# Kernel tuning notes

Measured on AMD Instinct MI355X. Metric: run time of the kernel, lower is better.

Reference implementation:

```python
import jax, jax.numpy as jnp
import numpy as np

TOP_K = 2  # num_experts_per_tok


def setup_inputs() -> dict:
    key = jax.random.key(0)
    k1, k2, k3, k4 = jax.random.split(key, 4)
    T, H, I, E = 1024, 2048, 768, 8  # tokens, hidden, moe_intermediate, num_experts
    return {
        "hidden_states": jax.random.normal(k1, (T, H), jnp.float32),
        "gate_w": jax.random.normal(k2, (E, H), jnp.float32) * 0.02,      # router nn.Linear(H,E) weight
        "w_gate_up": jax.random.normal(k3, (E, 2 * I, H), jnp.float32) * 0.02,  # merged gate+up proj per expert
        "w_down": jax.random.normal(k4, (E, H, I), jnp.float32) * 0.02,   # down proj per expert
    }


def _moe(hidden_states, gate_w, w_gate_up, w_down):
    T, H = hidden_states.shape
    E = gate_w.shape[0]
    # router: softmax in fp32, then top-k, renormalize (matches _forward_local)
    logits = hidden_states @ gate_w.T                         # [T, E]
    probs = jax.nn.softmax(logits.astype(jnp.float32), axis=-1)
    top_w, top_i = jax.lax.top_k(probs, TOP_K)                # [T, K]
    top_w = top_w / jnp.sum(top_w, axis=-1, keepdims=True)
    top_w = top_w.astype(hidden_states.dtype)
    # per-token combine weight for each expert (top-k indices are unique per token)
    comb = jnp.zeros((T, E), hidden_states.dtype).at[
        jnp.arange(T)[:, None], top_i
    ].add(top_w)                                              # [T, E]

    def body(acc, xs):
        wgu, wd, cw = xs            # [2I,H], [H,I], [T]
        gu = hidden_states @ wgu.T  # [T, 2I]
        g, u = jnp.split(gu, 2, axis=-1)
        h = jax.nn.silu(g) * u      # SiluAndMul
        out = h @ wd.T              # [T, H]
        return acc + out * cw[:, None], None

    init = jnp.zeros_like(hidden_states)
    out, _ = jax.lax.scan(body, init, (w_gate_up, w_down, comb.T))
    return out


def reference(hidden_states, gate_w, w_gate_up, w_down):
    return _moe(hidden_states, gate_w, w_gate_up, w_down)
```

## Files before the change

### kernel.cpp

```cpp
#include <hip/hip_runtime.h>
#include <hip/hip_bf16.h>

typedef unsigned short u16;
typedef __bf16 bf16x8 __attribute__((ext_vector_type(8)));
typedef float f32x4 __attribute__((ext_vector_type(4)));

#define T_TOK 1024
#define HID   2048
#define IMM   768
#define NE    8
#define TWOI  1536

static __device__ __forceinline__ u16 f2bf(float f) {
  unsigned u = __float_as_uint(f);
  u += 0x7FFFu + ((u >> 16) & 1u);
  return (u16)(u >> 16);
}
static __device__ __forceinline__ float bf2f(u16 s) {
  return __uint_as_float(((unsigned)s) << 16);
}

__global__ __launch_bounds__(64) void router_kernel(
    const float* __restrict__ hid, const float* __restrict__ gw,
    int* __restrict__ cnt, int* __restrict__ tok_of, float* __restrict__ wslot)
{
  const int t = blockIdx.x;
  const int lane = threadIdx.x;
  float acc[NE];
#pragma unroll
  for (int e = 0; e < NE; ++e) acc[e] = 0.f;
  const float4* h4 = (const float4*)(hid + (long)t * HID);
#pragma unroll 2
  for (int c = lane; c < HID / 4; c += 64) {
    float4 x = h4[c];
#pragma unroll
    for (int e = 0; e < NE; ++e) {
      float4 w = ((const float4*)(gw + e * HID))[c];
      acc[e] += x.x * w.x + x.y * w.y + x.z * w.z + x.w * w.w;
    }
  }
#pragma unroll
  for (int e = 0; e < NE; ++e) {
    float v = acc[e];
#pragma unroll
    for (int off = 32; off > 0; off >>= 1) v += __shfl_xor(v, off, 64);
    acc[e] = v;
  }
  if (lane == 0) {
    float mx = acc[0];
#pragma unroll
    for (int e = 1; e < NE; ++e) mx = fmaxf(mx, acc[e]);
    float p[NE]; float s = 0.f;
#pragma unroll
    for (int e = 0; e < NE; ++e) { p[e] = expf(acc[e] - mx); s += p[e]; }
    const float inv = 1.f / s;
    float p1 = -1.f, p2 = -1.f; int i1 = 0, i2 = 0;
#pragma unroll
    for (int e = 0; e < NE; ++e) {
      float pe = p[e] * inv;
      if (pe > p1)      { p2 = p1; i2 = i1; p1 = pe; i1 = e; }
      else if (pe > p2) { p2 = pe; i2 = e; }
    }
    const float wsum = p1 + p2;
    int s1 = atomicAdd(&cnt[i1], 1);
    tok_of[i1 * T_TOK + s1] = t;
    wslot[i1 * T_TOK + s1] = p1 / wsum;
    int s2 = atomicAdd(&cnt[i2], 1);
    tok_of[i2 * T_TOK + s2] = t;
    wslot[i2 * T_TOK + s2] = p2 / wsum;
  }
}

__global__ __launch_bounds__(256) void cvt_kernel(
    const float* __restrict__ in, u16* __restrict__ out)
{
  const int i = blockIdx.x * 256 + threadIdx.x;
  float4 x = ((const float4*)in)[i];
  ushort4 o;
  o.x = f2bf(x.x); o.y = f2bf(x.y); o.z = f2bf(x.z); o.w = f2bf(x.w);
  ((ushort4*)out)[i] = o;
}

template<int K, int KS, bool GATHER_A, bool OUT_ATOMIC>
__global__ __launch_bounds__(256, 4) void gemm_moe(
    const u16* __restrict__ A, int lda, long a_zoff,
    const float* __restrict__ B, long b_zoff,
    const int* __restrict__ tok_of, const int* __restrict__ cnt,
    u16* __restrict__ Cb, long ks_coff, float* __restrict__ Cf,
    int ldc, long c_zoff)
{
  constexpr int BM = 128, BN = 128, BK = 32;
  constexpr int LSTR = BK + 8;
  constexpr int KH  = K / KS;
  constexpr int NKT = KH / BK;
  static_assert(NKT >= 2 && (KH % BK) == 0, "K chunk must be multiple of 32, >=64");

  const int z  = blockIdx.z;
  const int e  = z & (NE - 1);
  const int ks = z >> 3;
  const int kb = ks * KH;

  const int nrow = cnt[e];
  const long m0 = (long)blockIdx.x * BM;
  if (m0 >= nrow) return;

  __shared__ __align__(16) u16 As[2][BM * LSTR];
  __shared__ __align__(16) u16 Bs[2][BN * LSTR];

  const int tid  = threadIdx.x;
  const int lane = tid & 63;
  const int wave = tid >> 6;
  const int wm = wave >> 1, wn = wave & 1;
  const int lrow = lane & 15;
  const int lk   = (lane >> 4) << 3;

  const long n0 = (long)blockIdx.y * BN;
  const float* Bb = B + b_zoff * e + n0 * (long)K;

  const int r0  = tid >> 2;
  const int cs0 = (tid & 3) << 3;

  const u16 *ap0, *ap1;
  if constexpr (GATHER_A) {
    ap0 = A + (long)tok_of[e * T_TOK + m0 + r0] * lda + kb + cs0;
    ap1 = A + (long)tok_of[e * T_TOK + m0 + r0 + 64] * lda + kb + cs0;
  } else {
    ap0 = A + a_zoff * e + (m0 + r0) * (long)lda + kb + cs0;
    ap1 = ap0 + 64l * lda;
  }

  uint4 sa0, sa1; float4 sb0a, sb0b, sb1a, sb1b;

  auto gload = [&](int kk) {
    sa0 = *(const uint4*)(ap0 + kk);
    sa1 = *(const uint4*)(ap1 + kk);
    const float* bp = Bb + (long)r0 * K + kb + kk + cs0;
    sb0a = *(const float4*)bp;
    sb0b = *(const float4*)(bp + 4);
    sb1a = *(const float4*)(bp + 64l * K);
    sb1b = *(const float4*)(bp + 64l * K + 4);
  };
  auto packb = [&](const float4& f0, const float4& f1) -> uint4 {
    return make_uint4(
      (unsigned)f2bf(f0.x) | ((unsigned)f2bf(f0.y) << 16),
      (unsigned)f2bf(f0.z) | ((unsigned)f2bf(f0.w) << 16),
      (unsigned)f2bf(f1.x) | ((unsigned)f2bf(f1.y) << 16),
      (unsigned)f2bf(f1.z) | ((unsigned)f2bf(f1.w) << 16));
  };
  auto swrite = [&](int buf) {
    *(uint4*)&As[buf][r0 * LSTR + cs0]        = sa0;
    *(uint4*)&As[buf][(r0 + 64) * LSTR + cs0] = sa1;
    *(uint4*)&Bs[buf][r0 * LSTR + cs0]        = packb(sb0a, sb0b);
    *(uint4*)&Bs[buf][(r0 + 64) * LSTR + cs0] = packb(sb1a, sb1b);
  };

  f32x4 acc[4][4];
  const f32x4 zero4 = {0.f, 0.f, 0.f, 0.f};
#pragma unroll
  for (int m = 0; m < 4; ++m)
#pragma unroll
    for (int n = 0; n < 4; ++n) acc[m][n] = zero4;

  auto compute = [&](int buf) {
    bf16x8 af[4], bfr[4];
#pragma unroll
    for (int m = 0; m < 4; ++m)
      af[m] = *(const bf16x8*)&As[buf][(wm * 64 + m * 16 + lrow) * LSTR + lk];
#pragma unroll
    for (int n = 0; n < 4; ++n)
      bfr[n] = *(const bf16x8*)&Bs[buf][(wn * 64 + n * 16 + lrow) * LSTR + lk];
#pragma unroll
    for (int m = 0; m < 4; ++m)
#pragma unroll
      for (int n = 0; n < 4; ++n)
        acc[m][n] = __builtin_amdgcn_mfma_f32_16x16x32_bf16(af[m], bfr[n], acc[m][n], 0, 0, 0);
  };

  gload(0);
  swrite(0);
  __syncthreads();
  int cur = 0;
#pragma unroll 1
  for (int kt = 0; kt < NKT - 1; ++kt) {
    gload((kt + 1) * BK);
    compute(cur);
    swrite(cur ^ 1);
    __syncthreads();
    cur ^= 1;
  }
  compute(cur);

  const int rloc = wm * 64 + ((lane >> 4) << 2);
  const long cbase = n0 + wn * 64 + lrow;
  u16* CbE = Cb + c_zoff * e + (long)ks * ks_coff;
#pragma unroll
  for (int m = 0; m < 4; ++m) {
#pragma unroll
    for (int n = 0; n < 4; ++n) {
#pragma unroll
      for (int j = 0; j < 4; ++j) {
        const long slot = m0 + rloc + m * 16 + j;
        const long col = cbase + n * 16;
        if constexpr (OUT_ATOMIC) {
          if (slot < nrow) {
            const long tok = tok_of[e * T_TOK + slot];
            atomicAdd(Cf + tok * ldc + col, acc[m][n][j]);
          }
        } else {
          CbE[slot * ldc + col] = f2bf(acc[m][n][j]);
        }
      }
    }
  }
}

__global__ __launch_bounds__(256) void silu_kernel(
    const u16* __restrict__ gu, long part_stride, const float* __restrict__ wslot,
    u16* __restrict__ hp)
{
  const int c = blockIdx.x * 256 + threadIdx.x;
  const int idx = c << 3;
  const int g = idx / IMM;
  const int i0 = idx - g * IMM;
  const u16* gp0 = gu + (long)g * TWOI + i0;
  const u16* gp1 = gp0 + part_stride;
  uint4 gv0 = *(const uint4*)gp0;
  uint4 uv0 = *(const uint4*)(gp0 + IMM);
  uint4 gv1 = *(const uint4*)gp1;
  uint4 uv1 = *(const uint4*)(gp1 + IMM);
  const float cw = wslot[g];
  const unsigned* g0w = (const unsigned*)&gv0;
  const unsigned* u0w = (const unsigned*)&uv0;
  const unsigned* g1w = (const unsigned*)&gv1;
  const unsigned* u1w = (const unsigned*)&uv1;
  unsigned outw[4];
#pragma unroll
  for (int q = 0; q < 4; ++q) {
    float ga = bf2f((u16)(g0w[q] & 0xFFFFu)) + bf2f((u16)(g1w[q] & 0xFFFFu));
    float gb = bf2f((u16)(g0w[q] >> 16))     + bf2f((u16)(g1w[q] >> 16));
    float ua = bf2f((u16)(u0w[q] & 0xFFFFu)) + bf2f((u16)(u1w[q] & 0xFFFFu));
    float ub = bf2f((u16)(u0w[q] >> 16))     + bf2f((u16)(u1w[q] >> 16));
    float h0 = cw * ua * (ga / (1.f + __expf(-ga)));
    float h1 = cw * ub * (gb / (1.f + __expf(-gb)));
    outw[q] = (unsigned)f2bf(h0) | ((unsigned)f2bf(h1) << 16);
  }
  *(uint4*)(hp + (long)g * IMM + i0) = make_uint4(outw[0], outw[1], outw[2], outw[3]);
}

extern "C" void kernel_launch(void* const* d_in, const int* in_sizes, int n_in,
                              void* d_out, int out_size, void* d_ws, size_t ws_size,
                              hipStream_t stream) {
  const float* hid = (const float*)d_in[0];
  const float* gw  = (const float*)d_in[1];
  const float* wgu = (const float*)d_in[2];
  const float* wd  = (const float*)d_in[3];
  float* out = (float*)d_out;

  char* ws = (char*)d_ws;
  u16*   hidb   = (u16*)ws;
  int*   cnt    = (int*)(ws + (4l << 20));
  int*   tok_of = (int*)(ws + (4l << 20) + (1l << 12));
  float* wslot  = (float*)(ws + (4l << 20) + (1l << 12) + (1l << 15));
  u16*   gu     = (u16*)(ws + (4l << 20) + (1l << 17));
  const long GU_PART = (long)NE * T_TOK * TWOI;
  u16*   hp     = (u16*)(ws + (4l << 20) + (1l << 17) + 2 * GU_PART * 2);

  hipMemsetAsync(d_out, 0, (size_t)out_size * sizeof(float), stream);
  hipMemsetAsync(ws + (4l << 20), 0, (1l << 17), stream);

  router_kernel<<<T_TOK, 64, 0, stream>>>(hid, gw, cnt, tok_of, wslot);
  cvt_kernel<<<(T_TOK * HID / 4) / 256, 256, 0, stream>>>(hid, hidb);
  gemm_moe<HID, 2, true, false>
      <<<dim3(T_TOK / 128, TWOI / 128, NE * 2), 256, 0, stream>>>(
      hidb, HID, 0, wgu, (long)TWOI * HID,
      tok_of, cnt, gu, GU_PART, nullptr, TWOI, (long)T_TOK * TWOI);
  silu_kernel<<<(NE * T_TOK * IMM / 8) / 256, 256, 0, stream>>>(gu, GU_PART, wslot, hp);
  gemm_moe<IMM, 2, false, true>
      <<<dim3(T_TOK / 128, HID / 128, NE * 2), 256, 0, stream>>>(
      hp, IMM, (long)T_TOK * IMM, wd, (long)HID * IMM,
      tok_of, cnt, nullptr, 0, out, HID, 0);
}
```

Baseline: 432.3 us.

## Reshape MoE GEMM tiles to 256x64 with swizzled 1D grid and split-K 4

Changes the expert GEMM tile from 128x128 to 256x64, flattens the grid to 1D with a die-interleaving swizzle, and raises split-K from 2 to 4 when the workspace permits, generalizing the SiLU reduction over KS partials. The intent is better fp32 weight streaming and more parallel blocks over the sparse per-expert rows. In exchange, weight-tile reuse per A row drops, the A loads become per-row strided, and split-K 4 doubles the intermediate partial buffer traffic.

```diff
diff --git a/kernel.cpp b/kernel.cpp
--- a/kernel.cpp
+++ b/kernel.cpp
@@ -81,27 +81,35 @@
   ((ushort4*)out)[i] = o;
 }
 
-template<int K, int KS, bool GATHER_A, bool OUT_ATOMIC>
-__global__ __launch_bounds__(256, 4) void gemm_moe(
+template<int K, int KS, int NTILES, bool GATHER_A, bool OUT_ATOMIC>
+__global__ __launch_bounds__(256, 3) void gemm_moe(
     const u16* __restrict__ A, int lda, long a_zoff,
     const float* __restrict__ B, long b_zoff,
     const int* __restrict__ tok_of, const int* __restrict__ cnt,
     u16* __restrict__ Cb, long ks_coff, float* __restrict__ Cf,
     int ldc, long c_zoff)
 {
-  constexpr int BM = 128, BN = 128, BK = 32;
+  constexpr int BM = 256, BN = 64, BK = 32;
+  constexpr int MCAP = 4;
   constexpr int LSTR = BK + 8;
   constexpr int KH  = K / KS;
   constexpr int NKT = KH / BK;
-  static_assert(NKT >= 2 && (KH % BK) == 0, "K chunk must be multiple of 32, >=64");
-
-  const int z  = blockIdx.z;
-  const int e  = z & (NE - 1);
-  const int ks = z >> 3;
-  const int kb = ks * KH;
+  constexpr int TOTAL = MCAP * NTILES * NE * KS;
+  static_assert(NKT >= 2 && (KH % BK) == 0, "bad K chunk");
+  static_assert((TOTAL % 8) == 0, "swizzle needs total%8==0");
+
+  const int phys = blockIdx.x;
+  const int orig = (phys & 7) * (TOTAL / 8) + (phys >> 3);
+  const int mi   = orig & (MCAP - 1);
+  const int r1   = orig >> 2;
+  const int n_t  = r1 % NTILES;
+  const int z    = r1 / NTILES;
+  const int ks   = z % KS;
+  const int e    = z / KS;
+  const int kb   = ks * KH;
 
   const int nrow = cnt[e];
-  const long m0 = (long)blockIdx.x * BM;
+  const long m0 = (long)mi * BM;
   if (m0 >= nrow) return;
 
   __shared__ __align__(16) u16 As[2][BM * LSTR];
@@ -109,49 +117,36 @@
 
   const int tid  = threadIdx.x;
   const int lane = tid & 63;
-  const int wave = tid >> 6;
-  const int wm = wave >> 1, wn = wave & 1;
+  const int wm   = tid >> 6;
   const int lrow = lane & 15;
   const int lk   = (lane >> 4) << 3;
 
-  const long n0 = (long)blockIdx.y * BN;
-  const float* Bb = B + b_zoff * e + n0 * (long)K;
-
-  const int r0  = tid >> 2;
-  const int cs0 = (tid & 3) << 3;
-
-  const u16 *ap0, *ap1;
+  const long n0 = (long)n_t * BN;
+
+  const u16* ap;
   if constexpr (GATHER_A) {
-    ap0 = A + (long)tok_of[e * T_TOK + m0 + r0] * lda + kb + cs0;
-    ap1 = A + (long)tok_of[e * T_TOK + m0 + r0 + 64] * lda + kb + cs0;
+    ap = A + (long)tok_of[e * T_TOK + m0 + tid] * lda + kb;
   } else {
-    ap0 = A + a_zoff * e + (m0 + r0) * (long)lda + kb + cs0;
-    ap1 = ap0 + 64l * lda;
-  }
-
-  uint4 sa0, sa1; float4 sb0a, sb0b, sb1a, sb1b;
+    ap = A + a_zoff * e + (m0 + tid) * (long)lda + kb;
+  }
+  const float* bp = B + b_zoff * e + (n0 + (tid >> 2)) * (long)K + kb + (tid & 3) * 8;
+
+  uint4 sa0, sa1, sa2, sa3; float4 sb0, sb1;
 
   auto gload = [&](int kk) {
-    sa0 = *(const uint4*)(ap0 + kk);
-    sa1 = *(const uint4*)(ap1 + kk);
-    const float* bp = Bb + (long)r0 * K + kb + kk + cs0;
-    sb0a = *(const float4*)bp;
-    sb0b = *(const float4*)(bp + 4);
-    sb1a = *(const float4*)(bp + 64l * K);
-    sb1b = *(const float4*)(bp + 64l * K + 4);
-  };
-  auto packb = [&](const float4& f0, const float4& f1) -> uint4 {
-    return make_uint4(
-      (unsigned)f2bf(f0.x) | ((unsigned)f2bf(f0.y) << 16),
-      (unsigned)f2bf(f0.z) | ((unsigned)f2bf(f0.w) << 16),
-      (unsigned)f2bf(f1.x) | ((unsigned)f2bf(f1.y) << 16),
-      (unsigned)f2bf(f1.z) | ((unsigned)f2bf(f1.w) << 16));
+    const uint4* a4 = (const uint4*)(ap + kk);
+    sa0 = a4[0]; sa1 = a4[1]; sa2 = a4[2]; sa3 = a4[3];
+    sb0 = *(const float4*)(bp + kk);
+    sb1 = *(const float4*)(bp + kk + 4);
   };
   auto swrite = [&](int buf) {
-    *(uint4*)&As[buf][r0 * LSTR + cs0]        = sa0;
-    *(uint4*)&As[buf][(r0 + 64) * LSTR + cs0] = sa1;
-    *(uint4*)&Bs[buf][r0 * LSTR + cs0]        = packb(sb0a, sb0b);
-    *(uint4*)&Bs[buf][(r0 + 64) * LSTR + cs0] = packb(sb1a, sb1b);
+    uint4* aw = (uint4*)&As[buf][tid * LSTR];
+    aw[0] = sa0; aw[1] = sa1; aw[2] = sa2; aw[3] = sa3;
+    *(uint4*)&Bs[buf][(tid >> 2) * LSTR + (tid & 3) * 8] = make_uint4(
+      (unsigned)f2bf(sb0.x) | ((unsigned)f2bf(sb0.y) << 16),
+      (unsigned)f2bf(sb0.z) | ((unsigned)f2bf(sb0.w) << 16),
+      (unsigned)f2bf(sb1.x) | ((unsigned)f2bf(sb1.y) << 16),
+      (unsigned)f2bf(sb1.z) | ((unsigned)f2bf(sb1.w) << 16));
   };
 
   f32x4 acc[4][4];
@@ -162,18 +157,18 @@
     for (int n = 0; n < 4; ++n) acc[m][n] = zero4;
 
   auto compute = [&](int buf) {
-    bf16x8 af[4], bfr[4];
+    bf16x8 af[4], bfv[4];
 #pragma unroll
     for (int m = 0; m < 4; ++m)
       af[m] = *(const bf16x8*)&As[buf][(wm * 64 + m * 16 + lrow) * LSTR + lk];
 #pragma unroll
     for (int n = 0; n < 4; ++n)
-      bfr[n] = *(const bf16x8*)&Bs[buf][(wn * 64 + n * 16 + lrow) * LSTR + lk];
+      bfv[n] = *(const bf16x8*)&Bs[buf][(n * 16 + lrow) * LSTR + lk];
 #pragma unroll
     for (int m = 0; m < 4; ++m)
 #pragma unroll
       for (int n = 0; n < 4; ++n)
-        acc[m][n] = __builtin_amdgcn_mfma_f32_16x16x32_bf16(af[m], bfr[n], acc[m][n], 0, 0, 0);
+        acc[m][n] = __builtin_amdgcn_mfma_f32_16x16x32_bf16(af[m], bfv[n], acc[m][n], 0, 0, 0);
   };
 
   gload(0);
@@ -191,8 +186,8 @@
   compute(cur);
 
   const int rloc = wm * 64 + ((lane >> 4) << 2);
-  const long cbase = n0 + wn * 64 + lrow;
-  u16* CbE = Cb + c_zoff * e + (long)ks * ks_coff;
+  const long cbase = n0 + lrow;
+  u16* CbE = Cb + (long)ks * ks_coff + c_zoff * e;
 #pragma unroll
   for (int m = 0; m < 4; ++m) {
 #pragma unroll
@@ -214,6 +209,7 @@
   }
 }
 
+template<int KS>
 __global__ __launch_bounds__(256) void silu_kernel(
     const u16* __restrict__ gu, long part_stride, const float* __restrict__ wslot,
     u16* __restrict__ hp)
@@ -222,26 +218,30 @@
   const int idx = c << 3;
   const int g = idx / IMM;
   const int i0 = idx - g * IMM;
-  const u16* gp0 = gu + (long)g * TWOI + i0;
-  const u16* gp1 = gp0 + part_stride;
-  uint4 gv0 = *(const uint4*)gp0;
-  uint4 uv0 = *(const uint4*)(gp0 + IMM);
-  uint4 gv1 = *(const uint4*)gp1;
-  uint4 uv1 = *(const uint4*)(gp1 + IMM);
+  float gacc[8], uacc[8];
+#pragma unroll
+  for (int q = 0; q < 8; ++q) { gacc[q] = 0.f; uacc[q] = 0.f; }
+#pragma unroll
+  for (int p = 0; p < KS; ++p) {
+    const u16* gp = gu + (long)p * part_stride + (long)g * TWOI + i0;
+    uint4 gv = *(const uint4*)gp;
+    uint4 uv = *(const uint4*)(gp + IMM);
+    const unsigned* gw_ = (const unsigned*)&gv;
+    const unsigned* uw_ = (const unsigned*)&uv;
+#pragma unroll
+    for (int q = 0; q < 4; ++q) {
+      gacc[2 * q]     += bf2f((u16)(gw_[q] & 0xFFFFu));
+      gacc[2 * q + 1] += bf2f((u16)(gw_[q] >> 16));
+      uacc[2 * q]     += bf2f((u16)(uw_[q] & 0xFFFFu));
+      uacc[2 * q + 1] += bf2f((u16)(uw_[q] >> 16));
+    }
+  }
   const float cw = wslot[g];
-  const unsigned* g0w = (const unsigned*)&gv0;
-  const unsigned* u0w = (const unsigned*)&uv0;
-  const unsigned* g1w = (const unsigned*)&gv1;
-  const unsigned* u1w = (const unsigned*)&uv1;
   unsigned outw[4];
 #pragma unroll
   for (int q = 0; q < 4; ++q) {
-    float ga = bf2f((u16)(g0w[q] & 0xFFFFu)) + bf2f((u16)(g1w[q] & 0xFFFFu));
-    float gb = bf2f((u16)(g0w[q] >> 16))     + bf2f((u16)(g1w[q] >> 16));
-    float ua = bf2f((u16)(u0w[q] & 0xFFFFu)) + bf2f((u16)(u1w[q] & 0xFFFFu));
-    float ub = bf2f((u16)(u0w[q] >> 16))     + bf2f((u16)(u1w[q] >> 16));
-    float h0 = cw * ua * (ga / (1.f + __expf(-ga)));
-    float h1 = cw * ub * (gb / (1.f + __expf(-gb)));
+    float h0 = cw * uacc[2 * q]     * (gacc[2 * q]     / (1.f + __expf(-gacc[2 * q])));
+    float h1 = cw * uacc[2 * q + 1] * (gacc[2 * q + 1] / (1.f + __expf(-gacc[2 * q + 1])));
     outw[q] = (unsigned)f2bf(h0) | ((unsigned)f2bf(h1) << 16);
   }
   *(uint4*)(hp + (long)g * IMM + i0) = make_uint4(outw[0], outw[1], outw[2], outw[3]);
@@ -256,27 +256,47 @@
   const float* wd  = (const float*)d_in[3];
   float* out = (float*)d_out;
 
+  const long GU_PART = (long)NE * T_TOK * TWOI;
   char* ws = (char*)d_ws;
   u16*   hidb   = (u16*)ws;
   int*   cnt    = (int*)(ws + (4l << 20));
   int*   tok_of = (int*)(ws + (4l << 20) + (1l << 12));
   float* wslot  = (float*)(ws + (4l << 20) + (1l << 12) + (1l << 15));
   u16*   gu     = (u16*)(ws + (4l << 20) + (1l << 17));
-  const long GU_PART = (long)NE * T_TOK * TWOI;
-  u16*   hp     = (u16*)(ws + (4l << 20) + (1l << 17) + 2 * GU_PART * 2);
 
   hipMemsetAsync(d_out, 0, (size_t)out_size * sizeof(float), stream);
   hipMemsetAsync(ws + (4l << 20), 0, (1l << 17), stream);
 
   router_kernel<<<T_TOK, 64, 0, stream>>>(hid, gw, cnt, tok_of, wslot);
   cvt_kernel<<<(T_TOK * HID / 4) / 256, 256, 0, stream>>>(hid, hidb);
-  gemm_moe<HID, 2, true, false>
-      <<<dim3(T_TOK / 128, TWOI / 128, NE * 2), 256, 0, stream>>>(
-      hidb, HID, 0, wgu, (long)TWOI * HID,
-      tok_of, cnt, gu, GU_PART, nullptr, TWOI, (long)T_TOK * TWOI);
-  silu_kernel<<<(NE * T_TOK * IMM / 8) / 256, 256, 0, stream>>>(gu, GU_PART, wslot, hp);
-  gemm_moe<IMM, 2, false, true>
-      <<<dim3(T_TOK / 128, HID / 128, NE * 2), 256, 0, stream>>>(
-      hp, IMM, (long)T_TOK * IMM, wd, (long)HID * IMM,
-      tok_of, cnt, nullptr, 0, out, HID, 0);
-}
+
+  const size_t base = (4l << 20) + (1l << 17);
+  const size_t need4 = base + 4 * GU_PART * 2 + (long)NE * T_TOK * IMM * 2;
+  const bool ks4 = ws_size >= need4;
+
+  if (ks4) {
+    u16* hp = (u16*)(ws + base + 4 * GU_PART * 2);
+    gemm_moe<HID, 4, TWOI / 64, true, false>
+        <<<4 * (TWOI / 64) * NE * 4, 256, 0, stream>>>(
+        hidb, HID, 0, wgu, (long)TWOI * HID,
+        tok_of, cnt, gu, GU_PART, nullptr, TWOI, (long)T_TOK * TWOI);
+    silu_kernel<4><<<(NE * T_TOK * IMM / 8) / 256, 256, 0, stream>>>(
+        gu, GU_PART, wslot, hp);
+    gemm_moe<IMM, 4, HID / 64, false, true>
+        <<<4 * (HID / 64) * NE * 4, 256, 0, stream>>>(
+        hp, IMM, (long)T_TOK * IMM, wd, (long)HID * IMM,
+        tok_of, cnt, nullptr, 0, out, HID, 0);
+  } else {
+    u16* hp = (u16*)(ws + base + 2 * GU_PART * 2);
+    gemm_moe<HID, 2, TWOI / 64, true, false>
+        <<<4 * (TWOI / 64) * NE * 2, 256, 0, stream>>>(
+        hidb, HID, 0, wgu, (long)TWOI * HID,
+        tok_of, cnt, gu, GU_PART, nullptr, TWOI, (long)T_TOK * TWOI);
+    silu_kernel<2><<<(NE * T_TOK * IMM / 8) / 256, 256, 0, stream>>>(
+        gu, GU_PART, wslot, hp);
+    gemm_moe<IMM, 2, HID / 64, false, true>
+        <<<4 * (HID / 64) * NE * 2, 256, 0, stream>>>(
+        hp, IMM, (long)T_TOK * IMM, wd, (long)HID * IMM,
+        tok_of, cnt, nullptr, 0, out, HID, 0);
+  }
+}
```

Measured after the change: 678.1 us. 1.57x slower.
